# Performance work log

Hardware: AMD Instinct MI355X
Metric: run time of the kernel (lower is better)

Reference implementation:

```python
import jax, jax.numpy as jnp
import numpy as np

EPS = 1e-5

def layer_norm(x, w, b):
    mu = jnp.mean(x, axis=-1, keepdims=True)
    var = jnp.mean(jnp.square(x - mu), axis=-1, keepdims=True)
    return (x - mu) * jax.lax.rsqrt(var + EPS) * w + b

def setup_inputs() -> dict:
    key = jax.random.key(0)
    k1, k2, k3, k4, k5, k6 = jax.random.split(key, 6)
    d = 768
    q_x = jax.random.normal(k1, (1, 8, d), dtype=jnp.float32)
    kv_x = jax.random.normal(k2, (32, 196, d), dtype=jnp.float32)
    ln_q_w = 1.0 + 0.1 * jax.random.normal(k3, (d,), dtype=jnp.float32)
    ln_q_b = 0.1 * jax.random.normal(k4, (d,), dtype=jnp.float32)
    ln_kv_w = 1.0 + 0.1 * jax.random.normal(k5, (d,), dtype=jnp.float32)
    ln_kv_b = 0.1 * jax.random.normal(k6, (d,), dtype=jnp.float32)
    return {"q_x": q_x, "kv_x": kv_x, "ln_q_w": ln_q_w, "ln_q_b": ln_q_b,
            "ln_kv_w": ln_kv_w, "ln_kv_b": ln_kv_b}

def reference(q_x, kv_x, ln_q_w, ln_q_b, ln_kv_w, ln_kv_b):
    b, n_patch, d = kv_x.shape
    n_q = q_x.shape[1]
    # expanded q is identical across b^2 rows -> normalize the single copy
    qn = layer_norm(q_x, ln_q_w, ln_q_b)[0]          # (n_q, d)
    kvn = layer_norm(kv_x, ln_kv_w, ln_kv_b)         # (b, n_patch, d)
    # pairwise batch differences: (b, b, n_patch, d) -> (b^2, n_patch, d)
    kv_pair = (kvn[:, None] - kvn[None, :]).reshape(b * b, n_patch, d)
    scores = jnp.einsum('qd,pnd->pqn', qn, kv_pair) / jnp.sqrt(jnp.asarray(d, qn.dtype))
    attn = jax.nn.softmax(scores, axis=-1)           # (b^2, n_q, n_patch)
    values = jnp.einsum('pqn,pnd->pqd', attn, kv_pair)
    return values
```

## Files before the change

kernel.cpp:

```cpp
#include <hip/hip_runtime.h>
#include <math.h>

constexpr int D  = 768;
constexpr int NQ = 8;
constexpr int B  = 32;
constexpr int NP = 196;
constexpr int KT = 7;
constexpr int KP = KT * 32;
constexpr int TPAD = 776;
constexpr int NTOFF = 28;
constexpr int NTILES = 32;
constexpr float EPS = 1e-5f;
constexpr float INV_SQRT_D = 0.036084391824351615f;

typedef __attribute__((ext_vector_type(8))) short short8;
typedef __attribute__((ext_vector_type(4))) float f32x4;

__device__ __forceinline__ float wave_reduce_sum(float v) {
#pragma unroll
    for (int off = 32; off > 0; off >>= 1) v += __shfl_xor(v, off, 64);
    return v;
}
__device__ __forceinline__ float wave_reduce_max(float v) {
#pragma unroll
    for (int off = 32; off > 0; off >>= 1) v = fmaxf(v, __shfl_xor(v, off, 64));
    return v;
}

__device__ __forceinline__ unsigned short f2bf(float x) {
    union { float f; unsigned u; } c; c.f = x;
    unsigned r = c.u + 0x7fffu + ((c.u >> 16) & 1u);
    return (unsigned short)(r >> 16);
}

__global__ __launch_bounds__(256, 4) void kv_fused(const float* __restrict__ q_x,
                                                   const float* __restrict__ qw,
                                                   const float* __restrict__ qb,
                                                   const float* __restrict__ kv_x,
                                                   const float* __restrict__ kw,
                                                   const float* __restrict__ kb,
                                                   float* __restrict__ S,
                                                   unsigned short* __restrict__ kvTf) {
    const int b = blockIdx.x / 14;
    const int h = blockIdx.x % 14;
    const int kt = h >> 1;
    const int kgbase = (h & 1) * 2;
    const int tid = threadIdx.x, wave = tid >> 6, lane = tid & 63;
    __shared__ unsigned short tile[16][TPAD];
    __shared__ unsigned short qbf[8][TPAD];

    const bool live = (h * 16) < NP;

    float wv[12], bv[12];
#pragma unroll
    for (int c = 0; c < 12; ++c) { wv[c] = kw[lane + 64 * c]; bv[c] = kb[lane + 64 * c]; }

    if (live && wave < 4) {
        float wq[12], bq[12];
#pragma unroll
        for (int c = 0; c < 12; ++c) { wq[c] = qw[lane + 64 * c]; bq[c] = qb[lane + 64 * c]; }
        float v0[12], v1[12];
        float s0 = 0.f, t0 = 0.f, s1 = 0.f, t1 = 0.f;
        const int q0 = wave * 2, q1 = q0 + 1;
#pragma unroll
        for (int c = 0; c < 12; ++c) {
            v0[c] = q_x[q0 * D + lane + 64 * c];
            v1[c] = q_x[q1 * D + lane + 64 * c];
            s0 += v0[c]; t0 = fmaf(v0[c], v0[c], t0);
            s1 += v1[c]; t1 = fmaf(v1[c], v1[c], t1);
        }
#pragma unroll
        for (int off = 32; off > 0; off >>= 1) {
            s0 += __shfl_xor(s0, off, 64);
            s1 += __shfl_xor(s1, off, 64);
            t0 += __shfl_xor(t0, off, 64);
            t1 += __shfl_xor(t1, off, 64);
        }
        const float m0 = s0 * (1.0f / D), m1 = s1 * (1.0f / D);
        const float r0 = rsqrtf(t0 * (1.0f / D) - m0 * m0 + EPS);
        const float r1 = rsqrtf(t1 * (1.0f / D) - m1 * m1 + EPS);
#pragma unroll
        for (int c = 0; c < 12; ++c) {
            qbf[q0][lane + 64 * c] = f2bf((v0[c] - m0) * r0 * wq[c] + bq[c]);
            qbf[q1][lane + 64 * c] = f2bf((v1[c] - m1) * r1 * wq[c] + bq[c]);
        }
    }

    unsigned pk01[12], pk23[12];
#pragma unroll
    for (int b2 = 0; b2 < 2; ++b2) {
        const int nl0 = wave * 4 + 2 * b2;
        const int n0 = h * 16 + nl0, n1 = n0 + 1;
        const bool a0 = n0 < NP, a1 = n1 < NP;
        const float* x0 = kv_x + ((size_t)b * NP + n0) * D;
        const float* x1 = kv_x + ((size_t)b * NP + n1) * D;
        float v0[12], v1[12];
        float s0 = 0.f, t0 = 0.f, s1 = 0.f, t1 = 0.f;
#pragma unroll
        for (int c = 0; c < 12; ++c) {
            v0[c] = a0 ? x0[lane + 64 * c] : 0.f;
            v1[c] = a1 ? x1[lane + 64 * c] : 0.f;
            s0 += v0[c]; t0 = fmaf(v0[c], v0[c], t0);
            s1 += v1[c]; t1 = fmaf(v1[c], v1[c], t1);
        }
#pragma unroll
        for (int off = 32; off > 0; off >>= 1) {
            s0 += __shfl_xor(s0, off, 64);
            s1 += __shfl_xor(s1, off, 64);
            t0 += __shfl_xor(t0, off, 64);
            t1 += __shfl_xor(t1, off, 64);
        }
        const float m0 = s0 * (1.0f / D), m1 = s1 * (1.0f / D);
        const float r0 = rsqrtf(t0 * (1.0f / D) - m0 * m0 + EPS);
        const float r1 = rsqrtf(t1 * (1.0f / D) - m1 * m1 + EPS);
#pragma unroll
        for (int c = 0; c < 12; ++c) {
            const int d = lane + 64 * c;
            const unsigned short bf0 = a0 ? f2bf((v0[c] - m0) * r0 * wv[c] + bv[c]) : (unsigned short)0;
            const unsigned short bf1 = a1 ? f2bf((v1[c] - m1) * r1 * wv[c] + bv[c]) : (unsigned short)0;
            tile[nl0][d] = bf0;
            tile[nl0 + 1][d] = bf1;
            const unsigned packed = (unsigned)bf0 | ((unsigned)bf1 << 16);
            if (b2 == 0) pk01[c] = packed; else pk23[c] = packed;
        }
    }

    {
        const int kg = kgbase + (wave >> 1);
        const int eh = (wave & 1);
        const int dl = lane & 15;
#pragma unroll
        for (int c = 0; c < 12; ++c) {
            const int dt = (lane >> 4) + 4 * c;
            uint2 val; val.x = pk01[c]; val.y = pk23[c];
            *(uint2*)(kvTf + ((((size_t)b * 48 + dt) * KT + kt) * 64 + kg * 16 + dl) * 8 + eh * 4) = val;
        }
    }
    __syncthreads();

    if (live && wave == 0) {
        f32x4 s0 = {0.f, 0.f, 0.f, 0.f}, s1 = {0.f, 0.f, 0.f, 0.f};
        const int ar = lane & 15, akg = lane >> 4;
        const int qr = ar & 7;
#pragma unroll
        for (int k2 = 0; k2 < 24; k2 += 2) {
            s0 = __builtin_amdgcn_mfma_f32_16x16x32_bf16(
                *(const short8*)&tile[ar][k2 * 32 + akg * 8],
                *(const short8*)&qbf[qr][k2 * 32 + akg * 8], s0, 0, 0, 0);
            s1 = __builtin_amdgcn_mfma_f32_16x16x32_bf16(
                *(const short8*)&tile[ar][(k2 + 1) * 32 + akg * 8],
                *(const short8*)&qbf[qr][(k2 + 1) * 32 + akg * 8], s1, 0, 0, 0);
        }
        s0 = s0 + s1;
        const int q = lane & 15;
        if (q < NQ) {
#pragma unroll
            for (int reg = 0; reg < 4; ++reg) {
                const int n = h * 16 + akg * 4 + reg;
                if (n < NP) S[((size_t)b * NQ + q) * NP + n] = s0[reg] * INV_SQRT_D;
            }
        }
    }
}

__global__ __launch_bounds__(512) void aprep(const float* __restrict__ S,
                                             unsigned short* __restrict__ Abf) {
    const int u = blockIdx.x;
    int uu = u, i = 0;
    while (uu >= 31 - i) { uu -= 31 - i; ++i; }
    const int j = i + 1 + uu;

    const int tid = threadIdx.x, wave = tid >> 6, lane = tid & 63;
    __shared__ unsigned short lrow[16][KP];

    for (int jj = 0; jj < 2; ++jj) {
        const int r = wave * 2 + jj;
        const int dir = r >> 3, q = r & 7;
        const float* Sa = S + ((size_t)(dir ? j : i) * NQ + q) * NP;
        const float* Sb = S + ((size_t)(dir ? i : j) * NQ + q) * NP;
        float v[4];
        float m = -1e30f;
#pragma unroll
        for (int c = 0; c < 4; ++c) {
            const int n = lane + 64 * c;
            v[c] = (n < NP) ? (Sa[n] - Sb[n]) : -1e30f;
            m = fmaxf(m, v[c]);
        }
        m = wave_reduce_max(m);
        float e[4];
        float sum = 0.f;
#pragma unroll
        for (int c = 0; c < 4; ++c) {
            const int n = lane + 64 * c;
            e[c] = (n < NP) ? __expf(v[c] - m) : 0.f;
            sum += e[c];
        }
        sum = wave_reduce_sum(sum);
        const float rinv = 1.0f / sum;
#pragma unroll
        for (int c = 0; c < 4; ++c) {
            const int n = lane + 64 * c;
            if (n < KP) lrow[r][n] = (n < NP) ? f2bf(e[c] * rinv) : (unsigned short)0;
        }
    }
    __syncthreads();

    if (tid < 448) {
        const int kt = tid >> 6, slot = tid & 63;
        const int kg = slot >> 4, lr = slot & 15;
        const short8 vals = *(const short8*)(&lrow[lr][kt * 32 + kg * 8]);
        *(short8*)(Abf + (((size_t)u * KT + kt) * 64 + slot) * 8) = vals;
    }
}

__global__ __launch_bounds__(512, 4) void dgemm(const unsigned short* __restrict__ Abf,
                                                const unsigned short* __restrict__ kvTf,
                                                float* __restrict__ out) {
    const int bid = blockIdx.x;
    const int t = bid >> 4, cs = bid & 15;
    const int tid = threadIdx.x, wave = tid >> 6, lane = tid & 63;

    __shared__ unsigned short stg[2][8][3][64][8];

    const bool offd = (t < NTOFF);
    int gi = 0, gj = 0;
    if (offd) {
        int tt = t, a = 0;
        while (tt >= 7 - a) { tt -= 7 - a; ++a; }
        gi = a; gj = a + 1 + tt;
    }
    const int dbase = 8 * (t - NTOFF);

    int i0 = 0, j0 = 0, i1 = 0, j1 = 0;
    int p0i = 0, p0j = 0, p1i = 0, p1j = 0;
    bool compute = true;
    if (offd) {
        const int pi = wave >> 1, bh = wave & 1;
        i0 = 4 * gi + pi; j0 = 4 * gj + 2 * bh;
        i1 = i0;          j1 = j0 + 1;
        p0i = pi; p0j = 4 + 2 * bh; p1i = pi; p1j = p0j + 1;
    } else if (wave < 6) {
        const int g = wave / 3, k3 = wave - 3 * g;
        const int ea[6] = {0, 0, 0, 1, 1, 2}, eb[6] = {1, 2, 3, 2, 3, 3};
        const int e0 = 2 * k3, e1 = e0 + 1;
        p0i = 4 * g + ea[e0]; p0j = 4 * g + eb[e0];
        p1i = 4 * g + ea[e1]; p1j = 4 * g + eb[e1];
        i0 = dbase + p0i; j0 = dbase + p0j;
        i1 = dbase + p1i; j1 = dbase + p1j;
    } else {
        compute = false;
        const int zw = wave - 6;
#pragma unroll
        for (int t2 = 0; t2 < 4; ++t2) {
            const int ii = dbase + zw * 4 + t2;
            float* base = out + (size_t)(ii * B + ii) * NQ * D + cs * 48;
#pragma unroll
            for (int rep = 0; rep < 6; ++rep) {
                const int e = rep * 64 + lane;
                const int q = e / 48, c = e - q * 48;
                base[q * D + c] = 0.f;
            }
        }
    }

    short8 areg0[KT], areg1[KT];
    if (compute) {
        const int u0 = (i0 * (63 - i0)) / 2 + (j0 - i0 - 1);
        const int u1 = (i1 * (63 - i1)) / 2 + (j1 - i1 - 1);
        const unsigned short* Au0 = Abf + (size_t)u0 * KT * 512 + (size_t)lane * 8;
        const unsigned short* Au1 = Abf + (size_t)u1 * KT * 512 + (size_t)lane * 8;
#pragma unroll
        for (int kt = 0; kt < KT; ++kt) {
            areg0[kt] = *(const short8*)(Au0 + (size_t)kt * 512);
            areg1[kt] = *(const short8*)(Au1 + (size_t)kt * 512);
        }
    }

    const int sp = wave;
    const int sb = offd ? ((sp < 4) ? (4 * gi + sp) : (4 * gj + sp - 4)) : (dbase + sp);
    const unsigned short* gbase =
        kvTf + (((size_t)sb * 48 + cs * 3) * KT) * 512 + (size_t)lane * 8;

    f32x4 acc0[3], acc1[3];
#pragma unroll
    for (int nf = 0; nf < 3; ++nf) {
        f32x4 z = {0.f, 0.f, 0.f, 0.f};
        acc0[nf] = z; acc1[nf] = z;
    }

#pragma unroll
    for (int r = 0; r < 3; ++r)
        __builtin_amdgcn_global_load_lds(
            (const __attribute__((address_space(1))) void*)(gbase + ((size_t)r * KT) * 512),
            (__attribute__((address_space(3))) void*)(&stg[0][sp][r][0][0]), 16, 0, 0);
    __syncthreads();

    int buf = 0;
    for (int kt = 0; kt < KT; ++kt) {
        if (kt + 1 < KT) {
#pragma unroll
            for (int r = 0; r < 3; ++r)
                __builtin_amdgcn_global_load_lds(
                    (const __attribute__((address_space(1))) void*)(gbase + ((size_t)r * KT + kt + 1) * 512),
                    (__attribute__((address_space(3))) void*)(&stg[buf ^ 1][sp][r][0][0]), 16, 0, 0);
        }
        if (compute) {
            const short8 a0 = areg0[kt], a1 = areg1[kt];
            short8 na0, na1;
#pragma unroll
            for (int e = 0; e < 8; ++e) {
                na0[e] = (short)(a0[e] ^ (short)0x8000);
                na1[e] = (short)(a1[e] ^ (short)0x8000);
            }
            if (offd) {
#pragma unroll
                for (int nf = 0; nf < 3; ++nf) {
                    const short8 ki  = *(const short8*)(&stg[buf][p0i][nf][lane][0]);
                    const short8 kj0 = *(const short8*)(&stg[buf][p0j][nf][lane][0]);
                    const short8 kj1 = *(const short8*)(&stg[buf][p1j][nf][lane][0]);
                    acc0[nf] = __builtin_amdgcn_mfma_f32_16x16x32_bf16(a0,  ki,  acc0[nf], 0, 0, 0);
                    acc0[nf] = __builtin_amdgcn_mfma_f32_16x16x32_bf16(na0, kj0, acc0[nf], 0, 0, 0);
                    acc1[nf] = __builtin_amdgcn_mfma_f32_16x16x32_bf16(a1,  ki,  acc1[nf], 0, 0, 0);
                    acc1[nf] = __builtin_amdgcn_mfma_f32_16x16x32_bf16(na1, kj1, acc1[nf], 0, 0, 0);
                }
            } else {
#pragma unroll
                for (int nf = 0; nf < 3; ++nf) {
                    const short8 k0i = *(const short8*)(&stg[buf][p0i][nf][lane][0]);
                    const short8 k0j = *(const short8*)(&stg[buf][p0j][nf][lane][0]);
                    const short8 k1i = *(const short8*)(&stg[buf][p1i][nf][lane][0]);
                    const short8 k1j = *(const short8*)(&stg[buf][p1j][nf][lane][0]);
                    acc0[nf] = __builtin_amdgcn_mfma_f32_16x16x32_bf16(a0,  k0i, acc0[nf], 0, 0, 0);
                    acc0[nf] = __builtin_amdgcn_mfma_f32_16x16x32_bf16(na0, k0j, acc0[nf], 0, 0, 0);
                    acc1[nf] = __builtin_amdgcn_mfma_f32_16x16x32_bf16(a1,  k1i, acc1[nf], 0, 0, 0);
                    acc1[nf] = __builtin_amdgcn_mfma_f32_16x16x32_bf16(na1, k1j, acc1[nf], 0, 0, 0);
                }
            }
        }
        __syncthreads();
        buf ^= 1;
    }

    if (compute) {
        const int kgrp = lane >> 4, dl = lane & 15;
        const int colb = cs * 48 + dl;
#pragma unroll
        for (int pr = 0; pr < 2; ++pr) {
            const int i = pr ? i1 : i0, j = pr ? j1 : j0;
            const f32x4* acc = pr ? acc1 : acc0;
            const int pij = i * B + j, pji = j * B + i;
#pragma unroll
            for (int reg = 0; reg < 4; ++reg) {
                const int r = kgrp * 4 + reg;
                const int dirr = r >> 3, qq = r & 7;
                const int p = dirr ? pji : pij;
                const float sgn = dirr ? -1.f : 1.f;
                float* op = out + ((size_t)p * NQ + qq) * D + colb;
#pragma unroll
                for (int nf = 0; nf < 3; ++nf) op[nf * 16] = sgn * acc[nf][reg];
            }
        }
    }
}

extern "C" void kernel_launch(void* const* d_in, const int* in_sizes, int n_in,
                              void* d_out, int out_size, void* d_ws, size_t ws_size,
                              hipStream_t stream) {
    const float* q_x     = (const float*)d_in[0];
    const float* kv_x    = (const float*)d_in[1];
    const float* ln_q_w  = (const float*)d_in[2];
    const float* ln_q_b  = (const float*)d_in[3];
    const float* ln_kv_w = (const float*)d_in[4];
    const float* ln_kv_b = (const float*)d_in[5];
    float* out = (float*)d_out;

    float* ws = (float*)d_ws;
    float* S  = ws;
    unsigned short* kvTf = (unsigned short*)(ws + B * NQ * NP);
    unsigned short* Abf  = kvTf + (size_t)B * 48 * KT * 512;

    kv_fused<<<B * 14, 256, 0, stream>>>(q_x, ln_q_w, ln_q_b, kv_x, ln_kv_w, ln_kv_b, S, kvTf);
    aprep<<<(B * (B - 1)) / 2, 512, 0, stream>>>(S, Abf);
    dgemm<<<NTILES * 16, 512, 0, stream>>>(Abf, kvTf, out);
}
```

Before: 35.74 us.

## Fuse softmax prep into dgemm and defer normalization to epilogue

Removes the separate aprep kernel: each dgemm wave now computes the pairwise score differences, max and exponentials directly from S into bf16 MFMA A-fragments in registers. The 1/sum normalization moves to the epilogue via a lane shuffle, so the softmax is unnormalized during the GEMM. This drops one launch and the Abf round-trip through global memory. The cost is that softmax work is redone by all 16 column-slice blocks per pair tile, and the bf16 values are unnormalized exps, which changes rounding slightly.

After: 53.54 us. 1.5x slower.

```diff
diff --git a/kernel.cpp b/kernel.cpp
--- a/kernel.cpp
+++ b/kernel.cpp
@@ -6,7 +6,6 @@
 constexpr int B  = 32;
 constexpr int NP = 196;
 constexpr int KT = 7;
-constexpr int KP = KT * 32;
 constexpr int TPAD = 776;
 constexpr int NTOFF = 28;
 constexpr int NTILES = 32;
@@ -19,11 +18,6 @@
 __device__ __forceinline__ float wave_reduce_sum(float v) {
 #pragma unroll
     for (int off = 32; off > 0; off >>= 1) v += __shfl_xor(v, off, 64);
-    return v;
-}
-__device__ __forceinline__ float wave_reduce_max(float v) {
-#pragma unroll
-    for (int off = 32; off > 0; off >>= 1) v = fmaxf(v, __shfl_xor(v, off, 64));
     return v;
 }
 
@@ -163,57 +157,7 @@
     }
 }
 
-__global__ __launch_bounds__(512) void aprep(const float* __restrict__ S,
-                                             unsigned short* __restrict__ Abf) {
-    const int u = blockIdx.x;
-    int uu = u, i = 0;
-    while (uu >= 31 - i) { uu -= 31 - i; ++i; }
-    const int j = i + 1 + uu;
-
-    const int tid = threadIdx.x, wave = tid >> 6, lane = tid & 63;
-    __shared__ unsigned short lrow[16][KP];
-
-    for (int jj = 0; jj < 2; ++jj) {
-        const int r = wave * 2 + jj;
-        const int dir = r >> 3, q = r & 7;
-        const float* Sa = S + ((size_t)(dir ? j : i) * NQ + q) * NP;
-        const float* Sb = S + ((size_t)(dir ? i : j) * NQ + q) * NP;
-        float v[4];
-        float m = -1e30f;
-#pragma unroll
-        for (int c = 0; c < 4; ++c) {
-            const int n = lane + 64 * c;
-            v[c] = (n < NP) ? (Sa[n] - Sb[n]) : -1e30f;
-            m = fmaxf(m, v[c]);
-        }
-        m = wave_reduce_max(m);
-        float e[4];
-        float sum = 0.f;
-#pragma unroll
-        for (int c = 0; c < 4; ++c) {
-            const int n = lane + 64 * c;
-            e[c] = (n < NP) ? __expf(v[c] - m) : 0.f;
-            sum += e[c];
-        }
-        sum = wave_reduce_sum(sum);
-        const float rinv = 1.0f / sum;
-#pragma unroll
-        for (int c = 0; c < 4; ++c) {
-            const int n = lane + 64 * c;
-            if (n < KP) lrow[r][n] = (n < NP) ? f2bf(e[c] * rinv) : (unsigned short)0;
-        }
-    }
-    __syncthreads();
-
-    if (tid < 448) {
-        const int kt = tid >> 6, slot = tid & 63;
-        const int kg = slot >> 4, lr = slot & 15;
-        const short8 vals = *(const short8*)(&lrow[lr][kt * 32 + kg * 8]);
-        *(short8*)(Abf + (((size_t)u * KT + kt) * 64 + slot) * 8) = vals;
-    }
-}
-
-__global__ __launch_bounds__(512, 4) void dgemm(const unsigned short* __restrict__ Abf,
+__global__ __launch_bounds__(512, 4) void dgemm(const float* __restrict__ S,
                                                 const unsigned short* __restrict__ kvTf,
                                                 float* __restrict__ out) {
     const int bid = blockIdx.x;
@@ -263,36 +207,82 @@
         }
     }
 
-    short8 areg0[KT], areg1[KT];
-    if (compute) {
-        const int u0 = (i0 * (63 - i0)) / 2 + (j0 - i0 - 1);
-        const int u1 = (i1 * (63 - i1)) / 2 + (j1 - i1 - 1);
-        const unsigned short* Au0 = Abf + (size_t)u0 * KT * 512 + (size_t)lane * 8;
-        const unsigned short* Au1 = Abf + (size_t)u1 * KT * 512 + (size_t)lane * 8;
-#pragma unroll
-        for (int kt = 0; kt < KT; ++kt) {
-            areg0[kt] = *(const short8*)(Au0 + (size_t)kt * 512);
-            areg1[kt] = *(const short8*)(Au1 + (size_t)kt * 512);
-        }
-    }
-
     const int sp = wave;
     const int sb = offd ? ((sp < 4) ? (4 * gi + sp) : (4 * gj + sp - 4)) : (dbase + sp);
     const unsigned short* gbase =
         kvTf + (((size_t)sb * 48 + cs * 3) * KT) * 512 + (size_t)lane * 8;
 
-    f32x4 acc0[3], acc1[3];
-#pragma unroll
-    for (int nf = 0; nf < 3; ++nf) {
-        f32x4 z = {0.f, 0.f, 0.f, 0.f};
-        acc0[nf] = z; acc1[nf] = z;
-    }
-
 #pragma unroll
     for (int r = 0; r < 3; ++r)
         __builtin_amdgcn_global_load_lds(
             (const __attribute__((address_space(1))) void*)(gbase + ((size_t)r * KT) * 512),
             (__attribute__((address_space(3))) void*)(&stg[0][sp][r][0][0]), 16, 0, 0);
+
+    short8 areg0[KT], areg1[KT];
+    float rinv0 = 1.f, rinv1 = 1.f;
+    if (compute) {
+        const int rr = lane & 15, kg = lane >> 4;
+        const int dir = rr >> 3, q = rr & 7;
+#pragma unroll
+        for (int pr = 0; pr < 2; ++pr) {
+            const int i = pr ? i1 : i0, j = pr ? j1 : j0;
+            const float* Sa = S + (size_t)((dir ? j : i) * NQ + q) * NP;
+            const float* Sb = S + (size_t)((dir ? i : j) * NQ + q) * NP;
+            float m = -1e30f;
+#pragma unroll
+            for (int kt = 0; kt < KT; ++kt) {
+                const int n0 = kt * 32 + kg * 8;
+                if (n0 < NP) {
+                    const f32x4 alo = *(const f32x4*)(Sa + n0);
+                    const f32x4 ahi = *(const f32x4*)(Sa + n0 + 4);
+                    const f32x4 blo = *(const f32x4*)(Sb + n0);
+                    const f32x4 bhi = *(const f32x4*)(Sb + n0 + 4);
+#pragma unroll
+                    for (int e = 0; e < 4; ++e) {
+                        if (n0 + e < NP)     m = fmaxf(m, alo[e] - blo[e]);
+                        if (n0 + 4 + e < NP) m = fmaxf(m, ahi[e] - bhi[e]);
+                    }
+                }
+            }
+            m = fmaxf(m, __shfl_xor(m, 16, 64));
+            m = fmaxf(m, __shfl_xor(m, 32, 64));
+            float sum = 0.f;
+#pragma unroll
+            for (int kt = 0; kt < KT; ++kt) {
+                const int n0 = kt * 32 + kg * 8;
+                short8 pk = {0, 0, 0, 0, 0, 0, 0, 0};
+                if (n0 < NP) {
+                    const f32x4 alo = *(const f32x4*)(Sa + n0);
+                    const f32x4 ahi = *(const f32x4*)(Sa + n0 + 4);
+                    const f32x4 blo = *(const f32x4*)(Sb + n0);
+                    const f32x4 bhi = *(const f32x4*)(Sb + n0 + 4);
+#pragma unroll
+                    for (int e = 0; e < 4; ++e) {
+                        if (n0 + e < NP) {
+                            const float ex = __expf(alo[e] - blo[e] - m);
+                            sum += ex; pk[e] = (short)f2bf(ex);
+                        }
+                        if (n0 + 4 + e < NP) {
+                            const float ex = __expf(ahi[e] - bhi[e] - m);
+                            sum += ex; pk[e + 4] = (short)f2bf(ex);
+                        }
+                    }
+                }
+                if (pr == 0) areg0[kt] = pk; else areg1[kt] = pk;
+            }
+            sum += __shfl_xor(sum, 16, 64);
+            sum += __shfl_xor(sum, 32, 64);
+            if (pr == 0) rinv0 = 1.0f / sum; else rinv1 = 1.0f / sum;
+        }
+    }
+
+    f32x4 acc0[3], acc1[3];
+#pragma unroll
+    for (int nf = 0; nf < 3; ++nf) {
+        f32x4 z = {0.f, 0.f, 0.f, 0.f};
+        acc0[nf] = z; acc1[nf] = z;
+    }
+
     __syncthreads();
 
     int buf = 0;
@@ -305,7 +295,11 @@
                     (__attribute__((address_space(3))) void*)(&stg[buf ^ 1][sp][r][0][0]), 16, 0, 0);
         }
         if (compute) {
-            const short8 a0 = areg0[kt], a1 = areg1[kt];
+            short8 a0, a1;
+#pragma unroll
+            for (int k2 = 0; k2 < KT; ++k2) {
+                if (k2 == kt) { a0 = areg0[k2]; a1 = areg1[k2]; }
+            }
             short8 na0, na1;
 #pragma unroll
             for (int e = 0; e < 8; ++e) {
@@ -348,16 +342,18 @@
         for (int pr = 0; pr < 2; ++pr) {
             const int i = pr ? i1 : i0, j = pr ? j1 : j0;
             const f32x4* acc = pr ? acc1 : acc0;
+            const float rinv = pr ? rinv1 : rinv0;
             const int pij = i * B + j, pji = j * B + i;
 #pragma unroll
             for (int reg = 0; reg < 4; ++reg) {
                 const int r = kgrp * 4 + reg;
+                const float rv = __shfl(rinv, r, 64);
                 const int dirr = r >> 3, qq = r & 7;
                 const int p = dirr ? pji : pij;
                 const float sgn = dirr ? -1.f : 1.f;
                 float* op = out + ((size_t)p * NQ + qq) * D + colb;
 #pragma unroll
-                for (int nf = 0; nf < 3; ++nf) op[nf * 16] = sgn * acc[nf][reg];
+                for (int nf = 0; nf < 3; ++nf) op[nf * 16] = sgn * rv * acc[nf][reg];
             }
         }
     }
@@ -377,9 +373,7 @@
     float* ws = (float*)d_ws;
     float* S  = ws;
     unsigned short* kvTf = (unsigned short*)(ws + B * NQ * NP);
-    unsigned short* Abf  = kvTf + (size_t)B * 48 * KT * 512;
 
     kv_fused<<<B * 14, 256, 0, stream>>>(q_x, ln_q_w, ln_q_b, kv_x, ln_kv_w, ln_kv_b, S, kvTf);
-    aprep<<<(B * (B - 1)) / 2, 512, 0, stream>>>(S, Abf);
-    dgemm<<<NTILES * 16, 512, 0, stream>>>(Abf, kvTf, out);
-}
+    dgemm<<<NTILES * 16, 512, 0, stream>>>(S, kvTf, out);
+}
```
